# Kernel optimization log

Hardware: AMD Instinct MI355X
Metric: run time of the kernel (lower is better)

## Reference

```python
import jax, jax.numpy as jnp
import numpy as np

H = 1024
N_HEAD = 16
HEAD = H // N_HEAD
EPS = 1e-12


def setup_inputs() -> dict:
    key = jax.random.key(0)
    ks = jax.random.split(key, 12)
    B, S = 2, 2048
    scale = 1.0 / np.sqrt(H)
    inp = {
        "pre_out": jax.random.normal(ks[0], (B, S, H), dtype=jnp.float32),
        "att_mask": jnp.ones((B, 1, 1, S), dtype=jnp.float32),
        "Wq": jax.random.normal(ks[1], (H, H), dtype=jnp.float32) * scale,
        "bq": jnp.zeros((H,), dtype=jnp.float32),
        "Wk": jax.random.normal(ks[2], (H, H), dtype=jnp.float32) * scale,
        "bk": jnp.zeros((H,), dtype=jnp.float32),
        "Wv": jax.random.normal(ks[3], (H, H), dtype=jnp.float32) * scale,
        "bv": jnp.zeros((H,), dtype=jnp.float32),
        "Wo": jax.random.normal(ks[4], (H, H), dtype=jnp.float32) * scale,
        "bo": jnp.zeros((H,), dtype=jnp.float32),
        "ln_w": jnp.ones((H,), dtype=jnp.float32),
        "ln_b": jnp.zeros((H,), dtype=jnp.float32),
    }
    return inp


def _heads(x):
    # [B,S,H] -> [B,n_head,S,head]
    B, S, _ = x.shape
    return x.reshape(B, S, N_HEAD, HEAD).transpose(0, 2, 1, 3)


def _layernorm(x, w, b):
    u = jnp.mean(x, axis=-1, keepdims=True)
    s = jnp.mean((x - u) ** 2, axis=-1, keepdims=True)
    return w * ((x - u) / jnp.sqrt(s + EPS)) + b


def reference(pre_out, att_mask, Wq, bq, Wk, bk, Wv, bv, Wo, bo, ln_w, ln_b):
    B, S, _ = pre_out.shape
    # torch Linear: y = x @ W.T + b
    Q = _heads(pre_out @ Wq.T + bq)
    K = _heads(pre_out @ Wk.T + bk)
    V = _heads(pre_out @ Wv.T + bv)
    scores = jnp.einsum('bhqd,bhkd->bhqk', Q, K) / np.sqrt(HEAD)
    scores = scores + (1.0 - att_mask) * -10000.0
    prob = jax.nn.softmax(scores, axis=-1)  # eval mode: no dropout
    att = jnp.einsum('bhqk,bhkd->bhqd', prob, V)
    att = att.transpose(0, 2, 1, 3).reshape(B, S, H)
    out = att @ Wo.T + bo
    return _layernorm(pre_out + out, ln_w, ln_b)
```

## Files before the change

kernel.cpp:

```cpp
#include <hip/hip_runtime.h>
#include <math.h>

typedef unsigned short u16;
typedef float floatx4 __attribute__((ext_vector_type(4)));
typedef __bf16 bf16x8 __attribute__((ext_vector_type(8)));
typedef u16 u16x4 __attribute__((ext_vector_type(4)));

#define BB 2
#define SS 2048
#define HH 1024
#define NHEAD 16

__device__ __forceinline__ u16 f2bf(float f) {
  union { float f; unsigned u; } a; a.f = f;
  unsigned r = a.u + 0x7fffu + ((a.u >> 16) & 1u);
  return (u16)(r >> 16);
}

__device__ __forceinline__ u16 bfbits(float f) {
  union { __bf16 h; u16 u; } c; c.h = (__bf16)f; return c.u;
}

__device__ __forceinline__ unsigned cvtpk(float lo, float hi) {
  unsigned r;
  asm("v_cvt_pk_bf16_f32 %0, %1, %2" : "=v"(r) : "v"(lo), "v"(hi));
  return r;
}

__device__ __forceinline__ void gload16(const u16* g, u16* l) {
  __builtin_amdgcn_global_load_lds((const __attribute__((address_space(1))) void*)g,
                                   (__attribute__((address_space(3))) void*)l, 16, 0, 0);
}

__device__ __forceinline__ void fencebar() {
  asm volatile("" ::: "memory");
  __builtin_amdgcn_s_barrier();
  asm volatile("" ::: "memory");
}

__global__ __launch_bounds__(256) void cvt_all(
    const float* __restrict__ X, const float* __restrict__ Wq, const float* __restrict__ Wk,
    const float* __restrict__ Wv, const float* __restrict__ Wo, const float* __restrict__ mask,
    u16* __restrict__ Xb, u16* __restrict__ Wqb, u16* __restrict__ Wkb,
    u16* __restrict__ Wvb, u16* __restrict__ Wob, float* __restrict__ B2) {
  int i = blockIdx.x * 256 + threadIdx.x;
  if (i >= (2 << 20)) {
    int off = i - (2 << 20);
    float4 m = ((const float4*)mask)[off];
    float4 o;
    o.x = (1.0f - m.x) * (-10000.0f * 1.44269504f);
    o.y = (1.0f - m.y) * (-10000.0f * 1.44269504f);
    o.z = (1.0f - m.z) * (-10000.0f * 1.44269504f);
    o.w = (1.0f - m.w) * (-10000.0f * 1.44269504f);
    ((float4*)B2)[off] = o;
    return;
  }
  const float* src; u16* dst; int off;
  if (i < (1 << 20)) { src = X; dst = Xb; off = i; }
  else {
    int j = i - (1 << 20);
    int m = j >> 18; off = j & ((1 << 18) - 1);
    src = (m == 0) ? Wq : (m == 1) ? Wk : (m == 2) ? Wv : Wo;
    dst = (m == 0) ? Wqb : (m == 1) ? Wkb : (m == 2) ? Wvb : Wob;
  }
  float4 v = ((const float4*)src)[off];
  u16x4 p; p.x = f2bf(v.x); p.y = f2bf(v.y); p.z = f2bf(v.z); p.w = f2bf(v.w);
  ((u16x4*)dst)[off] = p;
}

__global__ __launch_bounds__(256) void qkv_gemm(
    const u16* __restrict__ X,
    const u16* __restrict__ Wq, const u16* __restrict__ Wk, const u16* __restrict__ Wv,
    const float* __restrict__ bq, const float* __restrict__ bk, const float* __restrict__ bv,
    u16* __restrict__ Qo, u16* __restrict__ Ko, u16* __restrict__ Vt) {
  __shared__ u16 As[2][128 * 32];
  __shared__ u16 Ws[2][128 * 32];

  const int tid = threadIdx.x;
  const int w = tid >> 6, lane = tid & 63, quad = lane >> 4, l15 = lane & 15;
  const int L = blockIdx.y * 24 + blockIdx.x;
  const int wid = (L & 7) * 96 + (L >> 3);
  const int bx = wid % 24, by = wid / 24;
  const int mat = bx >> 3;
  const int col0 = (bx & 7) * 128;
  const int row0 = by * 128;
  const u16* W = (mat == 0) ? Wq : (mat == 1) ? Wk : Wv;
  const float* bias = (mat == 0) ? bq : (mat == 1) ? bk : bv;

  const int c0 = tid, c1 = tid + 256;
  const int ar0 = c0 >> 2, al0 = ((c0 & 3) ^ (ar0 & 3)) * 8;
  const int ar1 = c1 >> 2, al1 = ((c1 & 3) ^ (ar1 & 3)) * 8;
  const u16* gA0 = X + (row0 + ar0) * HH + al0;
  const u16* gA1 = X + (row0 + ar1) * HH + al1;
  const u16* gW0 = W + (col0 + ar0) * HH + al0;
  const u16* gW1 = W + (col0 + ar1) * HH + al1;

  const int wm = (w >> 1) * 64, wn = (w & 1) * 64;
  const int sw = quad ^ (l15 & 3);
  const int aoff = (wm + l15) * 32 + sw * 8;
  const int boff = (wn + l15) * 32 + sw * 8;

  auto stage = [&](int buf, int k0) {
    gload16(gA0 + k0, As[buf] + c0 * 8);
    gload16(gA1 + k0, As[buf] + c1 * 8);
    gload16(gW0 + k0, Ws[buf] + c0 * 8);
    gload16(gW1 + k0, Ws[buf] + c1 * 8);
  };

  floatx4 acc[4][4];
#pragma unroll
  for (int i = 0; i < 4; i++)
#pragma unroll
    for (int j = 0; j < 4; j++) acc[i][j] = {0.f, 0.f, 0.f, 0.f};

  stage(0, 0);

  for (int kt = 0; kt < 32; kt++) {
    const int cur = kt & 1;
    if (kt < 31) {
      stage(cur ^ 1, (kt + 1) * 32);
      asm volatile("s_waitcnt vmcnt(4)" ::: "memory");
    } else {
      asm volatile("s_waitcnt vmcnt(0)" ::: "memory");
    }
    fencebar();

    bf16x8 af[4], bfr[4];
#pragma unroll
    for (int i = 0; i < 4; i++) af[i] = *(const bf16x8*)(As[cur] + aoff + i * 512);
#pragma unroll
    for (int j = 0; j < 4; j++) bfr[j] = *(const bf16x8*)(Ws[cur] + boff + j * 512);
    __builtin_amdgcn_s_setprio(1);
#pragma unroll
    for (int i = 0; i < 4; i++)
#pragma unroll
      for (int j = 0; j < 4; j++)
        acc[i][j] = __builtin_amdgcn_mfma_f32_16x16x32_bf16(af[i], bfr[j], acc[i][j], 0, 0, 0);
    __builtin_amdgcn_s_setprio(0);

    fencebar();
  }

  const int rb = row0 + wm + quad * 4;
  if (mat < 2) {
    u16* O = (mat == 0) ? Qo : Ko;
#pragma unroll
    for (int j = 0; j < 4; j++) {
      const int col = col0 + wn + j * 16 + l15;
      const float bj = bias[col];
#pragma unroll
      for (int i = 0; i < 4; i++) {
        const int r0 = rb + i * 16;
#pragma unroll
        for (int r = 0; r < 4; r++)
          O[(r0 + r) * HH + col] = bfbits(acc[i][j][r] + bj);
      }
    }
  } else {
#pragma unroll
    for (int j = 0; j < 4; j++) {
      const int col = col0 + wn + j * 16 + l15;
      const float bj = bias[col];
      const int h = col >> 6, d = col & 63;
#pragma unroll
      for (int i = 0; i < 4; i++) {
        const int m0 = rb + i * 16;
        const int b = m0 >> 11, s = m0 & 2047;
        u16x4 pk;
#pragma unroll
        for (int r = 0; r < 4; r++) pk[r] = bfbits(acc[i][j][r] + bj);
        *(u16x4*)(Vt + (((b * NHEAD + h) * 64 + d) * SS + s)) = pk;
      }
    }
  }
}

__global__ __launch_bounds__(256) void oproj_gemm(
    const u16* __restrict__ A, const u16* __restrict__ W,
    const float* __restrict__ bias, float* __restrict__ Y) {
  __shared__ u16 As[2][128 * 32];
  __shared__ u16 Ws[2][64 * 32];

  const int tid = threadIdx.x;
  const int w = tid >> 6, lane = tid & 63, quad = lane >> 4, l15 = lane & 15;
  const int L = blockIdx.y * 16 + blockIdx.x;
  const int wid = (L & 7) * 64 + (L >> 3);
  const int col0 = (wid & 15) * 64;
  const int row0 = (wid >> 4) * 128;

  const int c0 = tid, c1 = tid + 256;
  const int ar0 = c0 >> 2, al0 = ((c0 & 3) ^ (ar0 & 3)) * 8;
  const int ar1 = c1 >> 2, al1 = ((c1 & 3) ^ (ar1 & 3)) * 8;
  const u16* gA0 = A + (row0 + ar0) * HH + al0;
  const u16* gA1 = A + (row0 + ar1) * HH + al1;
  const u16* gW0 = W + (col0 + ar0) * HH + al0;

  const int wm = w * 32;
  const int sw = quad ^ (l15 & 3);
  const int aoff = (wm + l15) * 32 + sw * 8;
  const int boff = l15 * 32 + sw * 8;

  auto stage = [&](int buf, int k0) {
    gload16(gA0 + k0, As[buf] + c0 * 8);
    gload16(gA1 + k0, As[buf] + c1 * 8);
    gload16(gW0 + k0, Ws[buf] + c0 * 8);
  };

  floatx4 acc[2][4];
#pragma unroll
  for (int i = 0; i < 2; i++)
#pragma unroll
    for (int j = 0; j < 4; j++) acc[i][j] = {0.f, 0.f, 0.f, 0.f};

  stage(0, 0);

  for (int kt = 0; kt < 32; kt++) {
    const int cur = kt & 1;
    if (kt < 31) {
      stage(cur ^ 1, (kt + 1) * 32);
      asm volatile("s_waitcnt vmcnt(3)" ::: "memory");
    } else {
      asm volatile("s_waitcnt vmcnt(0)" ::: "memory");
    }
    fencebar();

    bf16x8 af[2], bfr[4];
#pragma unroll
    for (int i = 0; i < 2; i++) af[i] = *(const bf16x8*)(As[cur] + aoff + i * 512);
#pragma unroll
    for (int j = 0; j < 4; j++) bfr[j] = *(const bf16x8*)(Ws[cur] + boff + j * 512);
    __builtin_amdgcn_s_setprio(1);
#pragma unroll
    for (int i = 0; i < 2; i++)
#pragma unroll
      for (int j = 0; j < 4; j++)
        acc[i][j] = __builtin_amdgcn_mfma_f32_16x16x32_bf16(af[i], bfr[j], acc[i][j], 0, 0, 0);
    __builtin_amdgcn_s_setprio(0);

    fencebar();
  }

  const int rb = row0 + wm + quad * 4;
#pragma unroll
  for (int j = 0; j < 4; j++) {
    const int col = col0 + j * 16 + l15;
    const float bj = bias[col];
#pragma unroll
    for (int i = 0; i < 2; i++) {
      const int r0 = rb + i * 16;
#pragma unroll
      for (int r = 0; r < 4; r++)
        Y[(r0 + r) * HH + col] = acc[i][j][r] + bj;
    }
  }
}

#define QT 128

__global__ __launch_bounds__(512, 4) void attn_mfma(
    const u16* __restrict__ Q, const u16* __restrict__ K, const u16* __restrict__ Vt,
    const float* __restrict__ B2, u16* __restrict__ O) {
  __shared__ u16 SMEM[24576];
  u16* const KB = SMEM;
  u16* const VB = SMEM + 12288;

  const int L = blockIdx.y * 16 + blockIdx.x;
  const int wid = (L & 7) * 64 + (L >> 3);
  const int qt = wid & 15, bh = wid >> 4;
  const int b = bh >> 4, h = bh & 15;
  const int tid = threadIdx.x;
  const int w = tid >> 6, lane = tid & 63, quad = lane >> 4, l15 = lane & 15;
  const int sw = l15 & 7;
  const int qg = w & 3;
  const int khalf = w >> 2;
  const int koff = khalf * 32;

  const int qbase  = (b * SS + qt * QT) * HH + h * 64;
  const int kvbase = (b * SS) * HH + h * 64;
  const int vtbase = (b * NHEAD + h) * 64 * SS;

  const int sr = tid >> 3, slc = (tid & 7) ^ (sr & 7);
  const u16* gKp = K + kvbase + sr * HH + slc * 8;
  const u16* gVp = Vt + vtbase + sr * SS + slc * 8;

  bf16x8 aQ[2][2];
#pragma unroll
  for (int mt = 0; mt < 2; mt++) {
    const u16* qr = Q + qbase + (qg * 32 + mt * 16 + l15) * HH;
    aQ[mt][0] = *(const bf16x8*)(qr + quad * 8);
    aQ[mt][1] = *(const bf16x8*)(qr + (4 + quad) * 8);
  }
  gload16(gKp, KB + tid * 8);
  gload16(gVp, VB + tid * 8);
  gload16(gKp + 64 * HH, KB + 4096 + tid * 8);
  gload16(gVp + 64, VB + 4096 + tid * 8);
  gKp += 2 * 64 * HH; gVp += 2 * 64;
  asm volatile("s_waitcnt vmcnt(2)" ::: "memory");

  floatx4 o[2][4];
#pragma unroll
  for (int mt = 0; mt < 2; mt++)
#pragma unroll
    for (int j = 0; j < 4; j++) o[mt][j] = {0.f, 0.f, 0.f, 0.f};
  float lp[2] = {0.f, 0.f};

  const float* B2p = B2 + b * SS + koff;

  const int krow0 = (koff + l15) * 64;
  const int kro0 = (quad ^ sw) * 8, kro1 = ((4 + quad) ^ sw) * 8;
  const int vc0 = khalf * 4 + (quad >> 1);
  const int vsub = (quad & 1) * 4;
  const int vo0 = (vc0 ^ sw) * 8 + vsub, vo1 = ((vc0 + 2) ^ sw) * 8 + vsub;

  int cOff = 0, nOff = 4096, sOff = 8192;

  for (int kt = 0; kt < 32; kt++) {
    fencebar();

    floatx4 bb[2];
    bb[0] = *(const floatx4*)(B2p + quad * 4);
    bb[1] = *(const floatx4*)(B2p + 16 + quad * 4);
    B2p += 64;
    asm volatile("" ::: "memory");

    if (kt < 30) {
      gload16(gKp, KB + sOff + tid * 8);
      gload16(gVp, VB + sOff + tid * 8);
      gKp += 64 * HH; gVp += 64;
      asm volatile("s_waitcnt vmcnt(2)" ::: "memory");
    } else {
      asm volatile("s_waitcnt vmcnt(0)" ::: "memory");
    }

    const u16* Kc = KB + cOff;
    const u16* Vc = VB + cOff;

    floatx4 st[2][2];
    __builtin_amdgcn_s_setprio(1);
#pragma unroll
    for (int kb = 0; kb < 2; kb++) {
      const u16* kr = Kc + krow0 + kb * 1024;
      bf16x8 kf0 = *(const bf16x8*)(kr + kro0);
      bf16x8 kf1 = *(const bf16x8*)(kr + kro1);
#pragma unroll
      for (int mt = 0; mt < 2; mt++) {
        floatx4 z = {0.f, 0.f, 0.f, 0.f};
        z = __builtin_amdgcn_mfma_f32_16x16x32_bf16(kf0, aQ[mt][0], z, 0, 0, 0);
        st[mt][kb] = __builtin_amdgcn_mfma_f32_16x16x32_bf16(kf1, aQ[mt][1], z, 0, 0, 0);
      }
    }
    __builtin_amdgcn_s_setprio(0);

    bf16x8 pa[2];
#pragma unroll
    for (int mt = 0; mt < 2; mt++) {
      float pe[2][4];
#pragma unroll
      for (int kb = 0; kb < 2; kb++)
#pragma unroll
        for (int r = 0; r < 4; r++) {
          pe[kb][r] = __builtin_amdgcn_exp2f(st[mt][kb][r] * 0.180336880f + bb[kb][r]);
          lp[mt] += pe[kb][r];
        }
      union { unsigned wd[4]; bf16x8 v; } pu;
      pu.wd[0] = cvtpk(pe[0][0], pe[0][1]);
      pu.wd[1] = cvtpk(pe[0][2], pe[0][3]);
      pu.wd[2] = cvtpk(pe[1][0], pe[1][1]);
      pu.wd[3] = cvtpk(pe[1][2], pe[1][3]);
      pa[mt] = pu.v;
    }

    __builtin_amdgcn_s_setprio(1);
#pragma unroll
    for (int j = 0; j < 4; j++) {
      const u16* vrow = Vc + (j * 16 + l15) * 64;
      union { u16x4 hh[2]; bf16x8 v; } vu;
      vu.hh[0] = *(const u16x4*)(vrow + vo0);
      vu.hh[1] = *(const u16x4*)(vrow + vo1);
#pragma unroll
      for (int mt = 0; mt < 2; mt++)
        o[mt][j] = __builtin_amdgcn_mfma_f32_16x16x32_bf16(pa[mt], vu.v, o[mt][j], 0, 0, 0);
    }
    __builtin_amdgcn_s_setprio(0);

    const int t = cOff; cOff = nOff; nOff = sOff; sOff = t;
  }

  fencebar();

#pragma unroll
  for (int mt = 0; mt < 2; mt++) {
    float v = lp[mt];
    v += __shfl_xor(v, 16);
    v += __shfl_xor(v, 32);
    lp[mt] = v;
  }

  float* const oS  = (float*)SMEM;
  float* const lpS = (float*)(SMEM + 16384);
  if (w >= 4) {
    float* pb = oS + (w - 4) * 2048;
#pragma unroll
    for (int mt = 0; mt < 2; mt++) {
#pragma unroll
      for (int j = 0; j < 4; j++)
#pragma unroll
        for (int r = 0; r < 4; r++)
          pb[(mt * 16 + quad * 4 + r) * 64 + j * 16 + l15] = o[mt][j][r];
      if (quad == 0) lpS[qg * 32 + mt * 16 + l15] = lp[mt];
    }
  }
  asm volatile("s_waitcnt lgkmcnt(0)" ::: "memory");
  fencebar();

  if (w < 4) {
    const float* pb = oS + w * 2048;
    float lpt[2];
#pragma unroll
    for (int mt = 0; mt < 2; mt++)
      lpt[mt] = lp[mt] + lpS[w * 32 + mt * 16 + l15];
#pragma unroll
    for (int mt = 0; mt < 2; mt++) {
      const int orow0 = b * SS + qt * QT + qg * 32 + mt * 16 + quad * 4;
#pragma unroll
      for (int r = 0; r < 4; r++) {
        const float inv = 1.0f / __shfl(lpt[mt], quad * 4 + r);
#pragma unroll
        for (int j = 0; j < 4; j++) {
          const float val = o[mt][j][r] + pb[(mt * 16 + quad * 4 + r) * 64 + j * 16 + l15];
          O[(orow0 + r) * HH + h * 64 + j * 16 + l15] = bfbits(val * inv);
        }
      }
    }
  }
}

__global__ __launch_bounds__(256) void add_layernorm(
    const float* __restrict__ x0, const float* __restrict__ y,
    const float* __restrict__ w, const float* __restrict__ b,
    float* __restrict__ out) {
  const int row = blockIdx.x * 4 + (threadIdx.x >> 6);
  const int l = threadIdx.x & 63;
  const float4* xr = (const float4*)(x0 + (size_t)row * HH);
  const float4* yr = (const float4*)(y + (size_t)row * HH);

  float4 v[4];
  float s = 0.f;
#pragma unroll
  for (int i = 0; i < 4; i++) {
    const float4 a = xr[l + i * 64];
    const float4 c = yr[l + i * 64];
    v[i].x = a.x + c.x; v[i].y = a.y + c.y;
    v[i].z = a.z + c.z; v[i].w = a.w + c.w;
    s += v[i].x + v[i].y + v[i].z + v[i].w;
  }
#pragma unroll
  for (int o = 1; o < 64; o <<= 1) s += __shfl_xor(s, o);
  const float mean = s * (1.0f / HH);

  float sq = 0.f;
#pragma unroll
  for (int i = 0; i < 4; i++) {
    const float dx = v[i].x - mean, dy = v[i].y - mean;
    const float dz = v[i].z - mean, dw = v[i].w - mean;
    sq += dx * dx + dy * dy + dz * dz + dw * dw;
  }
#pragma unroll
  for (int o = 1; o < 64; o <<= 1) sq += __shfl_xor(sq, o);
  const float inv = rsqrtf(sq * (1.0f / HH) + 1e-12f);

  float4* orow = (float4*)(out + (size_t)row * HH);
#pragma unroll
  for (int i = 0; i < 4; i++) {
    const float4 ww = ((const float4*)w)[l + i * 64];
    const float4 bb = ((const float4*)b)[l + i * 64];
    float4 o4;
    o4.x = ww.x * ((v[i].x - mean) * inv) + bb.x;
    o4.y = ww.y * ((v[i].y - mean) * inv) + bb.y;
    o4.z = ww.z * ((v[i].z - mean) * inv) + bb.z;
    o4.w = ww.w * ((v[i].w - mean) * inv) + bb.w;
    orow[l + i * 64] = o4;
  }
}

extern "C" void kernel_launch(void* const* d_in, const int* in_sizes, int n_in,
                              void* d_out, int out_size, void* d_ws, size_t ws_size,
                              hipStream_t stream) {
  const float* pre_out = (const float*)d_in[0];
  const float* mask    = (const float*)d_in[1];
  const float* Wq = (const float*)d_in[2];
  const float* bq = (const float*)d_in[3];
  const float* Wk = (const float*)d_in[4];
  const float* bk = (const float*)d_in[5];
  const float* Wv = (const float*)d_in[6];
  const float* bv = (const float*)d_in[7];
  const float* Wo = (const float*)d_in[8];
  const float* bo = (const float*)d_in[9];
  const float* ln_w = (const float*)d_in[10];
  const float* ln_b = (const float*)d_in[11];
  float* out = (float*)d_out;

  u16* Xb  = (u16*)d_ws;
  u16* Wqb = Xb + (4 << 20);
  u16* Wkb = Wqb + (1 << 20);
  u16* Wvb = Wkb + (1 << 20);
  u16* Wob = Wvb + (1 << 20);
  u16* Qb  = Wob + (1 << 20);
  u16* Kb  = Qb + (4 << 20);
  u16* Vtb = Kb + (4 << 20);
  u16* Ab  = Vtb + (4 << 20);
  float* Yb = (float*)(Ab + (4 << 20));
  float* B2 = Yb + (4 << 20);

  cvt_all<<<8196, 256, 0, stream>>>(pre_out, Wq, Wk, Wv, Wo, mask,
                                    Xb, Wqb, Wkb, Wvb, Wob, B2);

  qkv_gemm<<<dim3(24, 32), 256, 0, stream>>>(Xb, Wqb, Wkb, Wvb, bq, bk, bv, Qb, Kb, Vtb);

  attn_mfma<<<dim3(SS / QT, BB * NHEAD), 512, 0, stream>>>(Qb, Kb, Vtb, B2, Ab);

  oproj_gemm<<<dim3(16, 32), 256, 0, stream>>>(Ab, Wob, bo, Yb);

  add_layernorm<<<BB * SS / 4, 256, 0, stream>>>(pre_out, Yb, ln_w, ln_b, out);
}
```

Measured before the change: 205.5 us.

## Halve attention query tile and switch K/V staging to double buffering

New measurement: 233.3 us. 1.14x slower.

```diff
diff --git a/kernel.cpp b/kernel.cpp
--- a/kernel.cpp
+++ b/kernel.cpp
@@ -255,18 +255,18 @@
   }
 }
 
-#define QT 128
-
-__global__ __launch_bounds__(512, 4) void attn_mfma(
+#define QT 64
+
+__global__ __launch_bounds__(512, 2) void attn_mfma(
     const u16* __restrict__ Q, const u16* __restrict__ K, const u16* __restrict__ Vt,
     const float* __restrict__ B2, u16* __restrict__ O) {
-  __shared__ u16 SMEM[24576];
+  __shared__ u16 SMEM[16512];
   u16* const KB = SMEM;
-  u16* const VB = SMEM + 12288;
-
-  const int L = blockIdx.y * 16 + blockIdx.x;
-  const int wid = (L & 7) * 64 + (L >> 3);
-  const int qt = wid & 15, bh = wid >> 4;
+  u16* const VB = SMEM + 8192;
+
+  const int L = blockIdx.y * 32 + blockIdx.x;
+  const int wid = (L & 7) * 128 + (L >> 3);
+  const int qt = wid & 31, bh = wid >> 5;
   const int b = bh >> 4, h = bh & 15;
   const int tid = threadIdx.x;
   const int w = tid >> 6, lane = tid & 63, quad = lane >> 4, l15 = lane & 15;
@@ -283,26 +283,20 @@
   const u16* gKp = K + kvbase + sr * HH + slc * 8;
   const u16* gVp = Vt + vtbase + sr * SS + slc * 8;
 
-  bf16x8 aQ[2][2];
-#pragma unroll
-  for (int mt = 0; mt < 2; mt++) {
-    const u16* qr = Q + qbase + (qg * 32 + mt * 16 + l15) * HH;
-    aQ[mt][0] = *(const bf16x8*)(qr + quad * 8);
-    aQ[mt][1] = *(const bf16x8*)(qr + (4 + quad) * 8);
+  bf16x8 aQ[2];
+  {
+    const u16* qr = Q + qbase + (qg * 16 + l15) * HH;
+    aQ[0] = *(const bf16x8*)(qr + quad * 8);
+    aQ[1] = *(const bf16x8*)(qr + (4 + quad) * 8);
   }
   gload16(gKp, KB + tid * 8);
   gload16(gVp, VB + tid * 8);
-  gload16(gKp + 64 * HH, KB + 4096 + tid * 8);
-  gload16(gVp + 64, VB + 4096 + tid * 8);
-  gKp += 2 * 64 * HH; gVp += 2 * 64;
-  asm volatile("s_waitcnt vmcnt(2)" ::: "memory");
-
-  floatx4 o[2][4];
-#pragma unroll
-  for (int mt = 0; mt < 2; mt++)
-#pragma unroll
-    for (int j = 0; j < 4; j++) o[mt][j] = {0.f, 0.f, 0.f, 0.f};
-  float lp[2] = {0.f, 0.f};
+  gKp += 64 * HH; gVp += 64;
+
+  floatx4 o[4];
+#pragma unroll
+  for (int j = 0; j < 4; j++) o[j] = {0.f, 0.f, 0.f, 0.f};
+  float lp = 0.f;
 
   const float* B2p = B2 + b * SS + koff;
 
@@ -312,10 +306,8 @@
   const int vsub = (quad & 1) * 4;
   const int vo0 = (vc0 ^ sw) * 8 + vsub, vo1 = ((vc0 + 2) ^ sw) * 8 + vsub;
 
-  int cOff = 0, nOff = 4096, sOff = 8192;
-
   for (int kt = 0; kt < 32; kt++) {
-    fencebar();
+    const int cur = (kt & 1) * 4096;
 
     floatx4 bb[2];
     bb[0] = *(const floatx4*)(B2p + quad * 4);
@@ -323,52 +315,47 @@
     B2p += 64;
     asm volatile("" ::: "memory");
 
-    if (kt < 30) {
-      gload16(gKp, KB + sOff + tid * 8);
-      gload16(gVp, VB + sOff + tid * 8);
+    if (kt < 31) {
+      const int nxt = 4096 - cur;
+      gload16(gKp, KB + nxt + tid * 8);
+      gload16(gVp, VB + nxt + tid * 8);
       gKp += 64 * HH; gVp += 64;
       asm volatile("s_waitcnt vmcnt(2)" ::: "memory");
     } else {
       asm volatile("s_waitcnt vmcnt(0)" ::: "memory");
     }
-
-    const u16* Kc = KB + cOff;
-    const u16* Vc = VB + cOff;
-
-    floatx4 st[2][2];
+    fencebar();
+
+    const u16* Kc = KB + cur;
+    const u16* Vc = VB + cur;
+
+    floatx4 st[2];
     __builtin_amdgcn_s_setprio(1);
 #pragma unroll
     for (int kb = 0; kb < 2; kb++) {
       const u16* kr = Kc + krow0 + kb * 1024;
       bf16x8 kf0 = *(const bf16x8*)(kr + kro0);
       bf16x8 kf1 = *(const bf16x8*)(kr + kro1);
-#pragma unroll
-      for (int mt = 0; mt < 2; mt++) {
-        floatx4 z = {0.f, 0.f, 0.f, 0.f};
-        z = __builtin_amdgcn_mfma_f32_16x16x32_bf16(kf0, aQ[mt][0], z, 0, 0, 0);
-        st[mt][kb] = __builtin_amdgcn_mfma_f32_16x16x32_bf16(kf1, aQ[mt][1], z, 0, 0, 0);
+      floatx4 z = {0.f, 0.f, 0.f, 0.f};
+      z = __builtin_amdgcn_mfma_f32_16x16x32_bf16(kf0, aQ[0], z, 0, 0, 0);
+      st[kb] = __builtin_amdgcn_mfma_f32_16x16x32_bf16(kf1, aQ[1], z, 0, 0, 0);
+    }
+    __builtin_amdgcn_s_setprio(0);
+
+    float pe[2][4];
+#pragma unroll
+    for (int kb = 0; kb < 2; kb++)
+#pragma unroll
+      for (int r = 0; r < 4; r++) {
+        pe[kb][r] = __builtin_amdgcn_exp2f(st[kb][r] * 0.180336880f + bb[kb][r]);
+        lp += pe[kb][r];
       }
-    }
-    __builtin_amdgcn_s_setprio(0);
-
-    bf16x8 pa[2];
-#pragma unroll
-    for (int mt = 0; mt < 2; mt++) {
-      float pe[2][4];
-#pragma unroll
-      for (int kb = 0; kb < 2; kb++)
-#pragma unroll
-        for (int r = 0; r < 4; r++) {
-          pe[kb][r] = __builtin_amdgcn_exp2f(st[mt][kb][r] * 0.180336880f + bb[kb][r]);
-          lp[mt] += pe[kb][r];
-        }
-      union { unsigned wd[4]; bf16x8 v; } pu;
-      pu.wd[0] = cvtpk(pe[0][0], pe[0][1]);
-      pu.wd[1] = cvtpk(pe[0][2], pe[0][3]);
-      pu.wd[2] = cvtpk(pe[1][0], pe[1][1]);
-      pu.wd[3] = cvtpk(pe[1][2], pe[1][3]);
-      pa[mt] = pu.v;
-    }
+    union { unsigned wd[4]; bf16x8 v; } pu;
+    pu.wd[0] = cvtpk(pe[0][0], pe[0][1]);
+    pu.wd[1] = cvtpk(pe[0][2], pe[0][3]);
+    pu.wd[2] = cvtpk(pe[1][0], pe[1][1]);
+    pu.wd[3] = cvtpk(pe[1][2], pe[1][3]);
+    const bf16x8 pa = pu.v;
 
     __builtin_amdgcn_s_setprio(1);
 #pragma unroll
@@ -377,59 +364,42 @@
       union { u16x4 hh[2]; bf16x8 v; } vu;
       vu.hh[0] = *(const u16x4*)(vrow + vo0);
       vu.hh[1] = *(const u16x4*)(vrow + vo1);
-#pragma unroll
-      for (int mt = 0; mt < 2; mt++)
-        o[mt][j] = __builtin_amdgcn_mfma_f32_16x16x32_bf16(pa[mt], vu.v, o[mt][j], 0, 0, 0);
+      o[j] = __builtin_amdgcn_mfma_f32_16x16x32_bf16(pa, vu.v, o[j], 0, 0, 0);
     }
     __builtin_amdgcn_s_setprio(0);
 
-    const int t = cOff; cOff = nOff; nOff = sOff; sOff = t;
-  }
-
-  fencebar();
-
-#pragma unroll
-  for (int mt = 0; mt < 2; mt++) {
-    float v = lp[mt];
-    v += __shfl_xor(v, 16);
-    v += __shfl_xor(v, 32);
-    lp[mt] = v;
-  }
+    fencebar();
+  }
+
+  lp += __shfl_xor(lp, 16);
+  lp += __shfl_xor(lp, 32);
 
   float* const oS  = (float*)SMEM;
   float* const lpS = (float*)(SMEM + 16384);
+  fencebar();
   if (w >= 4) {
-    float* pb = oS + (w - 4) * 2048;
-#pragma unroll
-    for (int mt = 0; mt < 2; mt++) {
-#pragma unroll
-      for (int j = 0; j < 4; j++)
-#pragma unroll
-        for (int r = 0; r < 4; r++)
-          pb[(mt * 16 + quad * 4 + r) * 64 + j * 16 + l15] = o[mt][j][r];
-      if (quad == 0) lpS[qg * 32 + mt * 16 + l15] = lp[mt];
-    }
+    float* pb = oS + (w - 4) * 1024;
+#pragma unroll
+    for (int j = 0; j < 4; j++)
+#pragma unroll
+      for (int r = 0; r < 4; r++)
+        pb[(quad * 4 + r) * 64 + j * 16 + l15] = o[j][r];
+    if (quad == 0) lpS[qg * 16 + l15] = lp;
   }
   asm volatile("s_waitcnt lgkmcnt(0)" ::: "memory");
   fencebar();
 
   if (w < 4) {
-    const float* pb = oS + w * 2048;
-    float lpt[2];
-#pragma unroll
-    for (int mt = 0; mt < 2; mt++)
-      lpt[mt] = lp[mt] + lpS[w * 32 + mt * 16 + l15];
-#pragma unroll
-    for (int mt = 0; mt < 2; mt++) {
-      const int orow0 = b * SS + qt * QT + qg * 32 + mt * 16 + quad * 4;
-#pragma unroll
-      for (int r = 0; r < 4; r++) {
-        const float inv = 1.0f / __shfl(lpt[mt], quad * 4 + r);
-#pragma unroll
-        for (int j = 0; j < 4; j++) {
-          const float val = o[mt][j][r] + pb[(mt * 16 + quad * 4 + r) * 64 + j * 16 + l15];
-          O[(orow0 + r) * HH + h * 64 + j * 16 + l15] = bfbits(val * inv);
-        }
+    const float* pb = oS + w * 1024;
+    const float lpt = lp + lpS[w * 16 + l15];
+    const int orow0 = b * SS + qt * QT + qg * 16 + quad * 4;
+#pragma unroll
+    for (int r = 0; r < 4; r++) {
+      const float inv = 1.0f / __shfl(lpt, quad * 4 + r);
+#pragma unroll
+      for (int j = 0; j < 4; j++) {
+        const float val = o[j][r] + pb[(quad * 4 + r) * 64 + j * 16 + l15];
+        O[(orow0 + r) * HH + h * 64 + j * 16 + l15] = bfbits(val * inv);
       }
     }
   }
```
